# Kernel optimization log

Measured on AMD Instinct MI355X. Metric: run time of the kernel, lower is better.

Reference implementation:

```python
import jax, jax.numpy as jnp
import numpy as np

D = 256; H = 4; DK = D // H
MAX_ATOMS = 13; EDGE_NUM = 78; PAD = 799; K = 20
PREFIX = MAX_ATOMS * 2 + 2 + EDGE_NUM * 4   # 340, tokens that get positional encoding
SEQ = PREFIX + K                             # 360
NPAIR = EDGE_NUM + MAX_ATOMS                 # 91 atom pairs (i,j), j up to max_atoms
DFF = 2048; MSP = 800; B = 256

# ---- static pair / gather index tables (numpy, computed once) ----
def _pairs():
    pi, pj, pe = [], [], []
    for i in range(MAX_ATOMS):
        base = sum(MAX_ATOMS - jj - 1 for jj in range(i))  # getEdgeIdx prefix
        for j in range(i + 1, MAX_ATOMS + 1):
            pi.append(i); pj.append(j); pe.append(base + (j - i) - 1)
    return np.array(pi), np.array(pj), np.array(pe)

PI, PJ, PEI = _pairs()
_eb = MAX_ATOMS * 2 + 2 + 2 * PEI           # edge feature start in encoder output (stride 2)
GIDX = np.stack([2*PI, 2*PI+1, 2*PJ, 2*PJ+1, _eb, _eb+1, _eb+2, _eb+3], axis=1)  # (91,8)
ZMASK = np.ones((NPAIR, 8), np.float32)
ZMASK[PJ == MAX_ATOMS, 4:] = 0.0            # j == max_atoms -> edge slots zeroed
ES = (MAX_ATOMS + 1) * 2 + 4 * PEI          # edge slice start in raw src (stride 4)
EIDX = ES[:, None] + np.arange(4)[None, :]  # (91,4)

def _pe_table():
    pe = np.zeros((PREFIX, D), np.float32)
    pos = np.arange(PREFIX, dtype=np.float64)[:, None]
    ev = np.arange(0, D, 2)
    pe[:, ev] = np.sin(pos / 10000.0 ** (2 * ev / D))
    pe[:, ev + 1] = np.cos(pos / 10000.0 ** (2 * (ev + 1) / D))
    return jnp.asarray(pe)

PETAB = _pe_table()

def _norm(x, a, b):
    mu = x.mean(-1, keepdims=True)
    sd = x.std(-1, keepdims=True, ddof=1)   # torch std is unbiased
    return a * (x - mu) / (sd + 1e-6) + b

def _out_mask(src):
    # vectorized get_pad_mask10; later conditions override earlier ones
    ai = src[:, 2*PI + 1]; aj = src[:, 2*PJ + 1]
    ti = src[:, 2*PI];     tj = src[:, 2*PJ]
    c1 = (ai == 2) | (aj == 2)                                  # -> [0,0,1]
    c2 = (tj == 1) | (ai == 1) | (aj == 1)                      # -> [0,1,1]
    c3 = (ti == PAD) | (tj == PAD) | (ai == 0) | (aj == 0)      # -> [1,1,1]
    c4 = jnp.asarray(PJ < MAX_ATOMS)[None, :] & jnp.any(src[:, EIDX] == 1, axis=-1)
    m111 = c3 | c4
    return jnp.stack([m111, m111 | c2, m111 | c2 | c1], axis=-1)  # (B,91,3) bool


def setup_inputs() -> dict:
    key = jax.random.key(0)
    ks = jax.random.split(key, 12)
    g = lambda k, shape, s=0.02: jax.random.normal(k, shape, jnp.float32) * s
    emb = g(ks[0], (MSP, D), 1.0).at[PAD].set(0.0)  # nn.Embedding zeroes padding row
    return {
        'src': jax.random.randint(ks[1], (B, SEQ), 0, MSP, dtype=jnp.int32),
        'emb': emb,
        'wq': g(ks[2], (D, D)), 'bq': jnp.zeros((D,), jnp.float32),
        'wk': g(ks[3], (D, D)), 'bk': jnp.zeros((D,), jnp.float32),
        'wv': g(ks[4], (D, D)), 'bv': jnp.zeros((D,), jnp.float32),
        'wo': g(ks[5], (D, D)), 'bo': jnp.zeros((D,), jnp.float32),
        'n1a': jnp.ones((D,), jnp.float32), 'n1b': jnp.zeros((D,), jnp.float32),
        'n2a': jnp.ones((D,), jnp.float32), 'n2b': jnp.zeros((D,), jnp.float32),
        'w1': g(ks[6], (D, DFF)), 'b1': jnp.zeros((DFF,), jnp.float32),
        'w2': g(ks[7], (DFF, D)), 'b2': jnp.zeros((D,), jnp.float32),
        'wl': g(ks[8], (8 * D, 3)), 'bl': jnp.zeros((3,), jnp.float32),
    }


def reference(src, emb, wq, bq, wk, bk, wv, bv, wo, bo, n1a, n1b, n2a, n2b,
              w1, b1, w2, b2, wl, bl):
    Bn, S = src.shape
    x = emb[src]                                             # (B,S,D)
    # positional encoding (scale + PE) only on first PREFIX tokens, dropout=eval/no-op
    xp = x[:, :PREFIX] * jnp.sqrt(jnp.float32(D)) + PETAB
    x = jnp.concatenate([xp, x[:, PREFIX:]], axis=1)
    pad = src != PAD                                         # (B,S) query-row mask
    # encoder layer (pre-norm, residual)
    x2 = _norm(x, n1a, n1b)
    def heads(w, b):
        return (x2 @ w + b).reshape(Bn, S, H, DK).transpose(0, 2, 1, 3)
    q, kk, v = heads(wq, bq), heads(wk, bk), heads(wv, bv)
    sc = jnp.einsum('bhqd,bhkd->bhqk', q, kk) / jnp.sqrt(jnp.float32(DK))
    sc = jnp.where(pad[:, None, :, None], sc, jnp.float32(-1e9))  # mask broadcasts over keys
    ctx = jnp.einsum('bhqk,bhkd->bhqd', jax.nn.softmax(sc, axis=-1), v)
    x = x + ctx.transpose(0, 2, 1, 3).reshape(Bn, S, D) @ wo + bo
    x2 = _norm(x, n2a, n2b)
    x = x + jax.nn.relu(x2 @ w1 + b1) @ w2 + b2
    # triangular atom-pair gather + concat, vectorized via static index table
    feat = x[:, GIDX] * jnp.asarray(ZMASK)[None, :, :, None]  # (B,91,8,D)
    logits = feat.reshape(Bn, NPAIR, 8 * D) @ wl + bl         # (B,91,3)
    return jnp.where(_out_mask(src), jnp.float32(-1e9), logits)
```

## Files before the change

kernel.cpp:

```cpp
#include <hip/hip_runtime.h>
#include <hip/hip_bf16.h>
#include <math.h>


using bf16 = __hip_bfloat16;
typedef __attribute__((ext_vector_type(4))) float f32x4;
typedef __attribute__((ext_vector_type(16))) float f32x16;
typedef long long i64;
typedef unsigned char uchar;

static __device__ __forceinline__ float wave_sum64(float v){
  #pragma unroll
  for (int o = 32; o >= 1; o >>= 1) v += __shfl_xor(v, o, 64);
  return v;
}

static __device__ __forceinline__ void gl_lds16(const void* g, void* l){
  __builtin_amdgcn_global_load_lds((const __attribute__((address_space(1))) void*)g,
                                   (__attribute__((address_space(3))) void*)l, 16, 0, 0);
}

static __device__ __forceinline__ unsigned pack2(float a, float b){
  union { bf16 h[2]; unsigned u; } u;
  u.h[0] = __float2bfloat16(a); u.h[1] = __float2bfloat16(b);
  return u.u;
}

static __device__ __forceinline__ uchar f2f8(float v){
  return (uchar)(__builtin_amdgcn_cvt_pk_fp8_f32(v, 0.f, 0, false) & 0xff);
}
static __device__ __forceinline__ unsigned pack4_fp8(float a, float b, float c, float d){
  int v = __builtin_amdgcn_cvt_pk_fp8_f32(a, b, 0, false);
  v = __builtin_amdgcn_cvt_pk_fp8_f32(c, d, v, true);
  return (unsigned)v;
}

static __device__ __forceinline__ float fexp2(float x){
  float r;
  asm("v_exp_f32 %0, %1" : "=v"(r) : "v"(x));
  return r;
}

__global__ __launch_bounds__(256) void cvt_all(
    const float* s0, const float* s1, const float* s2, const float* s3,
    const float* s4, const float* s5,
    uchar* d0, uchar* d1, uchar* d2, uchar* d3, uchar* d4, uchar* d5)
{
  __shared__ float t[32][33];
  const float* srcs[6] = {s0, s1, s2, s3, s4, s5};
  uchar* dsts[6] = {d0, d1, d2, d3, d4, d5};
  const int Ks[6] = {256, 256, 256, 256, 256, 2048};
  const int Ns[6] = {256, 256, 256, 256, 2048, 256};
  const int offs[7] = {0, 64, 128, 192, 256, 768, 1280};
  int bid = blockIdx.x, j = 5;
  #pragma unroll
  for (int q = 4; q >= 0; q--) if (bid < offs[q + 1]) j = q;
  int local = bid - offs[j];
  int K = Ks[j], N = Ns[j];
  const float* src = srcs[j];
  uchar* dst = dsts[j];
  int kt = K >> 5;
  int kb = (local % kt) * 32, nb = (local / kt) * 32;
  int tx = threadIdx.x & 31, ty = threadIdx.x >> 5;
  #pragma unroll
  for (int dy = 0; dy < 32; dy += 8)
    t[ty + dy][tx] = src[(size_t)(kb + ty + dy) * N + nb + tx];
  __syncthreads();
  #pragma unroll
  for (int dy = 0; dy < 32; dy += 8)
    dst[(size_t)(nb + ty + dy) * K + kb + tx] = f2f8(t[tx][ty + dy]);
}

__global__ __launch_bounds__(256) void embed_ln1(
    const int* __restrict__ src, const float* __restrict__ emb,
    const float* __restrict__ na, const float* __restrict__ nb,
    bf16* __restrict__ x, uchar* __restrict__ xn8)
{
  int row  = blockIdx.x * 4 + (threadIdx.x >> 6);
  int lane = threadIdx.x & 63;
  int s = row % 360;
  int tok = src[row];
  float4 v = *(const float4*)(emb + (size_t)tok * 256 + lane * 4);
  float vv[4] = {v.x, v.y, v.z, v.w};
  if (s < 340){
    const float C = (-2.0f / 256.0f) * 13.287712379549449f;
    #pragma unroll
    for (int t = 0; t < 4; t++){
      int c = lane * 4 + t;
      float ang = (float)s * exp2f(C * (float)c);
      float pe = (c & 1) ? cosf(ang) : sinf(ang);
      vv[t] = 16.0f * vv[t] + pe;
    }
  }
  float sum = wave_sum64(vv[0] + vv[1] + vv[2] + vv[3]);
  float mu = sum * (1.0f / 256.0f);
  float d0 = vv[0]-mu, d1 = vv[1]-mu, d2 = vv[2]-mu, d3 = vv[3]-mu;
  float sq = wave_sum64(d0*d0 + d1*d1 + d2*d2 + d3*d3);
  float inv = 1.0f / (sqrtf(sq * (1.0f / 255.0f)) + 1e-6f);
  bf16 xo[4] = { __float2bfloat16(vv[0]), __float2bfloat16(vv[1]),
                 __float2bfloat16(vv[2]), __float2bfloat16(vv[3]) };
  *(uint2*)(x + (size_t)row * 256 + lane * 4) = *(uint2*)xo;
  float4 a4 = *(const float4*)(na + lane * 4);
  float4 b4 = *(const float4*)(nb + lane * 4);
  unsigned u = pack4_fp8(a4.x * d0 * inv + b4.x, a4.y * d1 * inv + b4.y,
                         a4.z * d2 * inv + b4.z, a4.w * d3 * inv + b4.w);
  *(unsigned*)(xn8 + (size_t)row * 256 + lane * 4) = u;
}

__global__ __launch_bounds__(256) void ln_k8(
    const bf16* __restrict__ x, const float* __restrict__ na,
    const float* __restrict__ nb, uchar* __restrict__ xn8)
{
  int row  = blockIdx.x * 4 + (threadIdx.x >> 6);
  int lane = threadIdx.x & 63;
  uint2 raw = *(const uint2*)(x + (size_t)row * 256 + lane * 4);
  bf16* xr = (bf16*)&raw;
  float v0 = __bfloat162float(xr[0]), v1 = __bfloat162float(xr[1]);
  float v2 = __bfloat162float(xr[2]), v3 = __bfloat162float(xr[3]);
  float sum = wave_sum64(v0 + v1 + v2 + v3);
  float mu = sum * (1.0f / 256.0f);
  float d0 = v0-mu, d1 = v1-mu, d2 = v2-mu, d3 = v3-mu;
  float sq = wave_sum64(d0*d0 + d1*d1 + d2*d2 + d3*d3);
  float inv = 1.0f / (sqrtf(sq * (1.0f / 255.0f)) + 1e-6f);
  float4 a4 = *(const float4*)(na + lane * 4);
  float4 b4 = *(const float4*)(nb + lane * 4);
  unsigned u = pack4_fp8(a4.x * d0 * inv + b4.x, a4.y * d1 * inv + b4.y,
                         a4.z * d2 * inv + b4.z, a4.w * d3 * inv + b4.w);
  *(unsigned*)(xn8 + (size_t)row * 256 + lane * 4) = u;
}

template<int MODE>
__global__ __launch_bounds__(256) void gemm_k256(
    const uchar* __restrict__ A, const uchar* __restrict__ Bt,
    const float* __restrict__ bias,
    uchar* __restrict__ out8, bf16* __restrict__ xres,
    int N, int nTiles,
    const float* __restrict__ bq, const float* __restrict__ bk)
{
  __shared__ __align__(16) char smem[65536];
  uchar* As = (uchar*)smem;
  uchar* Bs = (uchar*)(smem + 32768);
  uchar* S8 = (uchar*)smem;
  bf16 (*Cs)[136] = (bf16 (*)[136])smem;
  int chunk = gridDim.x >> 3;
  int bi = (blockIdx.x & 7) * chunk + (blockIdx.x >> 3);
  int m0 = (bi / nTiles) * 128, n0 = (bi % nTiles) * 128;
  int tid = threadIdx.x;
  int wave = tid >> 6, lane = tid & 63;
  int wm = (wave >> 1) * 64, wn = (wave & 1) * 64;
  int r32 = lane & 31, half = lane >> 5;

  #pragma unroll
  for (int j = 0; j < 8; j++){
    int c = j * 256 + tid;
    int row = c >> 4, p = c & 15;
    int sl = (p & 8) | ((p & 7) ^ (row & 7));
    gl_lds16(A  + (size_t)(m0 + row) * 256 + sl * 16, As + (size_t)c * 16);
    gl_lds16(Bt + (size_t)(n0 + row) * 256 + sl * 16, Bs + (size_t)c * 16);
  }

  f32x16 acc[2][2];
  #pragma unroll
  for (int mb = 0; mb < 2; mb++)
    #pragma unroll
    for (int nb = 0; nb < 2; nb++)
      #pragma unroll
      for (int e = 0; e < 16; e++) acc[mb][nb][e] = 0.f;

  __syncthreads();

  #pragma unroll
  for (int c = 0; c < 8; c++){
    int l0 = 2 * c + half;
    i64 alo[2], ahi[2], blo[2], bhi[2];
    #pragma unroll
    for (int mb = 0; mb < 2; mb++){
      int row = wm + mb * 32 + r32;
      int st = (l0 & 8) | ((l0 & 7) ^ (row & 7));
      uint4 v = *(const uint4*)(As + row * 256 + st * 16);
      alo[mb] = *(const i64*)&v.x;  ahi[mb] = *(const i64*)&v.z;
    }
    #pragma unroll
    for (int nb = 0; nb < 2; nb++){
      int row = wn + nb * 32 + r32;
      int st = (l0 & 8) | ((l0 & 7) ^ (row & 7));
      uint4 v = *(const uint4*)(Bs + row * 256 + st * 16);
      blo[nb] = *(const i64*)&v.x;  bhi[nb] = *(const i64*)&v.z;
    }
    #pragma unroll
    for (int mb = 0; mb < 2; mb++)
      #pragma unroll
      for (int nb = 0; nb < 2; nb++){
        if (MODE == 5){
          acc[mb][nb] = __builtin_amdgcn_mfma_f32_32x32x16_fp8_fp8(alo[mb], blo[nb], acc[mb][nb], 0, 0, 0);
          acc[mb][nb] = __builtin_amdgcn_mfma_f32_32x32x16_fp8_fp8(ahi[mb], bhi[nb], acc[mb][nb], 0, 0, 0);
        } else {
          acc[mb][nb] = __builtin_amdgcn_mfma_f32_32x32x16_fp8_fp8(blo[nb], alo[mb], acc[mb][nb], 0, 0, 0);
          acc[mb][nb] = __builtin_amdgcn_mfma_f32_32x32x16_fp8_fp8(bhi[nb], ahi[mb], acc[mb][nb], 0, 0, 0);
        }
      }
  }

  __syncthreads();

  if (MODE == 2 || MODE == 4){
    const int region = (MODE == 4) ? (n0 >> 8) : 0;
    const float* bb = (MODE == 4) ? (region == 0 ? bq : bk) : bias;
    #pragma unroll
    for (int mb = 0; mb < 2; mb++){
      int m_l = wm + mb * 32 + r32;
      #pragma unroll
      for (int nb = 0; nb < 2; nb++)
        #pragma unroll
        for (int g = 0; g < 4; g++){
          int n_l = wn + nb * 32 + g * 8 + half * 4;
          int bidx = (MODE == 4) ? ((n0 & 255) + n_l) : (n0 + n_l);
          float v0 = acc[mb][nb][g * 4 + 0] + bb[bidx + 0];
          float v1 = acc[mb][nb][g * 4 + 1] + bb[bidx + 1];
          float v2 = acc[mb][nb][g * 4 + 2] + bb[bidx + 2];
          float v3 = acc[mb][nb][g * 4 + 3] + bb[bidx + 3];
          if (MODE == 2){
            v0 = fmaxf(v0, 0.f); v1 = fmaxf(v1, 0.f);
            v2 = fmaxf(v2, 0.f); v3 = fmaxf(v3, 0.f);
          }
          *(unsigned*)(S8 + m_l * 136 + n_l) = pack4_fp8(v0, v1, v2, v3);
        }
    }
    __syncthreads();
    int lr = tid >> 1, seg = tid & 1;
    #pragma unroll
    for (int j = 0; j < 4; j++){
      int nl = seg * 64 + j * 16;
      uint2 a = *(uint2*)(S8 + lr * 136 + nl);
      uint2 b = *(uint2*)(S8 + lr * 136 + nl + 8);
      uint4 st = make_uint4(a.x, a.y, b.x, b.y);
      if (MODE == 2){
        *(uint4*)(out8 + (size_t)(m0 + lr) * N + n0 + nl) = st;
      } else {
        int m = m0 + lr;
        int b_ = m / 360, s = m - b_ * 360;
        int nnl = (n0 & 255) + nl;
        int h = nnl >> 6, dk = nnl & 63;
        size_t roff = (region == 1) ? 23592960ull : 0ull;
        *(uint4*)(out8 + roff + ((size_t)(b_ * 4 + h) * 360 + s) * 64 + dk) = st;
      }
    }
  } else if (MODE == 5){
    #pragma unroll
    for (int nb = 0; nb < 2; nb++){
      int n_l = wn + nb * 32 + r32;
      float bv_ = bias[n0 + n_l];
      #pragma unroll
      for (int mb = 0; mb < 2; mb++)
        #pragma unroll
        for (int g = 0; g < 4; g++){
          int m_l = wm + mb * 32 + g * 8 + half * 4;
          *(unsigned*)(S8 + n_l * 136 + m_l) =
              pack4_fp8(acc[mb][nb][g * 4 + 0] + bv_, acc[mb][nb][g * 4 + 1] + bv_,
                        acc[mb][nb][g * 4 + 2] + bv_, acc[mb][nb][g * 4 + 3] + bv_);
        }
    }
    __syncthreads();
    int nn = tid >> 1, part = tid & 1;
    int nnl = n0 + nn;
    int h = nnl >> 6, dk = nnl & 63;
    #pragma unroll
    for (int j0 = 0; j0 < 64; j0 += 8){
      int mm = m0 + part * 64 + j0;
      int b_ = mm / 360, s = mm - b_ * 360;
      uint2 val = *(uint2*)(S8 + nn * 136 + part * 64 + j0);
      *(uint2*)(out8 + ((size_t)((b_ * 4 + h) * 64 + dk)) * 360 + s) = val;
    }
  } else {
    #pragma unroll
    for (int hb = 0; hb < 2; hb++){
      if ((wave >> 1) == hb){
        #pragma unroll
        for (int mb = 0; mb < 2; mb++){
          int ml = mb * 32 + r32;
          #pragma unroll
          for (int nb = 0; nb < 2; nb++)
            #pragma unroll
            for (int g = 0; g < 4; g++){
              int nl0 = wn + nb * 32 + g * 8 + half * 4;
              float v0 = acc[mb][nb][g * 4 + 0] + bias[n0 + nl0 + 0];
              float v1 = acc[mb][nb][g * 4 + 1] + bias[n0 + nl0 + 1];
              float v2 = acc[mb][nb][g * 4 + 2] + bias[n0 + nl0 + 2];
              float v3 = acc[mb][nb][g * 4 + 3] + bias[n0 + nl0 + 3];
              *(unsigned*)(&Cs[ml][nl0])     = pack2(v0, v1);
              *(unsigned*)(&Cs[ml][nl0 + 2]) = pack2(v2, v3);
            }
        }
      }
      __syncthreads();
      int mbase = m0 + hb * 64;
      int lr = tid >> 2, seg = tid & 3;
      bf16* op = xres + (size_t)(mbase + lr) * 256 + n0 + seg * 32;
      #pragma unroll
      for (int j = 0; j < 4; j++){
        uint4 cv = *(uint4*)(&Cs[lr][seg * 32 + j * 8]);
        uint4 xv = *(uint4*)(op + j * 8);
        bf16* ca = (bf16*)&cv; bf16* xa = (bf16*)&xv;
        bf16 o8[8];
        #pragma unroll
        for (int t = 0; t < 8; t++)
          o8[t] = __float2bfloat16(__bfloat162float(ca[t]) + __bfloat162float(xa[t]));
        *(uint4*)(op + j * 8) = *(uint4*)o8;
      }
      __syncthreads();
    }
  }
}

__global__ __launch_bounds__(256) void gemm_ffn2(
    const uchar* __restrict__ A, const uchar* __restrict__ Bt,
    const float* __restrict__ bias, bf16* __restrict__ xres,
    int nTiles)
{
  __shared__ __align__(16) char smem[65536];
  bf16 (*Cs)[136] = (bf16 (*)[136])smem;
  int chunk = gridDim.x >> 3;
  int bi = (blockIdx.x & 7) * chunk + (blockIdx.x >> 3);
  int m0 = (bi / nTiles) * 128, n0 = (bi % nTiles) * 128;
  int tid = threadIdx.x;
  int wave = tid >> 6, lane = tid & 63;
  int wm = (wave >> 1) * 64, wn = (wave & 1) * 64;
  int r32 = lane & 31, half = lane >> 5;

  const uchar* ag[4]; const uchar* bg[4]; int ldst[4];
  #pragma unroll
  for (int j = 0; j < 4; j++){
    int c = j * 256 + tid;
    int row = c >> 3, p = c & 7;
    int sl = p ^ (row & 7);
    ag[j] = A  + (size_t)(m0 + row) * 2048 + sl * 16;
    bg[j] = Bt + (size_t)(n0 + row) * 2048 + sl * 16;
    ldst[j] = c * 16;
  }

  f32x16 acc[2][2];
  #pragma unroll
  for (int mb = 0; mb < 2; mb++)
    #pragma unroll
    for (int nb = 0; nb < 2; nb++)
      #pragma unroll
      for (int e = 0; e < 16; e++) acc[mb][nb][e] = 0.f;

  #pragma unroll
  for (int j = 0; j < 4; j++){
    gl_lds16(ag[j], (uchar*)smem + ldst[j]);
    gl_lds16(bg[j], (uchar*)smem + 32768 + ldst[j]);
  }
  __syncthreads();

  int cur = 0;
  for (int t = 0; t < 16; t++){
    int nxt = cur ^ 1;
    if (t < 15){
      #pragma unroll
      for (int j = 0; j < 4; j++){
        gl_lds16(ag[j] + (t + 1) * 128, (uchar*)smem + nxt * 16384 + ldst[j]);
        gl_lds16(bg[j] + (t + 1) * 128, (uchar*)smem + 32768 + nxt * 16384 + ldst[j]);
      }
    }
    const uchar* Ac = (const uchar*)smem + cur * 16384;
    const uchar* Bc = (const uchar*)smem + 32768 + cur * 16384;
    #pragma unroll
    for (int c = 0; c < 4; c++){
      int l0 = 2 * c + half;
      i64 alo[2], ahi[2], blo[2], bhi[2];
      #pragma unroll
      for (int mb = 0; mb < 2; mb++){
        int row = wm + mb * 32 + r32;
        int st = l0 ^ (row & 7);
        uint4 v = *(const uint4*)(Ac + row * 128 + st * 16);
        alo[mb] = *(const i64*)&v.x;  ahi[mb] = *(const i64*)&v.z;
      }
      #pragma unroll
      for (int nb = 0; nb < 2; nb++){
        int row = wn + nb * 32 + r32;
        int st = l0 ^ (row & 7);
        uint4 v = *(const uint4*)(Bc + row * 128 + st * 16);
        blo[nb] = *(const i64*)&v.x;  bhi[nb] = *(const i64*)&v.z;
      }
      #pragma unroll
      for (int mb = 0; mb < 2; mb++)
        #pragma unroll
        for (int nb = 0; nb < 2; nb++){
          acc[mb][nb] = __builtin_amdgcn_mfma_f32_32x32x16_fp8_fp8(blo[nb], alo[mb], acc[mb][nb], 0, 0, 0);
          acc[mb][nb] = __builtin_amdgcn_mfma_f32_32x32x16_fp8_fp8(bhi[nb], ahi[mb], acc[mb][nb], 0, 0, 0);
        }
    }
    __syncthreads();
    cur ^= 1;
  }

  #pragma unroll
  for (int hb = 0; hb < 2; hb++){
    if ((wave >> 1) == hb){
      #pragma unroll
      for (int mb = 0; mb < 2; mb++){
        int ml = mb * 32 + r32;
        #pragma unroll
        for (int nb = 0; nb < 2; nb++)
          #pragma unroll
          for (int g = 0; g < 4; g++){
            int nl0 = wn + nb * 32 + g * 8 + half * 4;
            float v0 = acc[mb][nb][g * 4 + 0] + bias[n0 + nl0 + 0];
            float v1 = acc[mb][nb][g * 4 + 1] + bias[n0 + nl0 + 1];
            float v2 = acc[mb][nb][g * 4 + 2] + bias[n0 + nl0 + 2];
            float v3 = acc[mb][nb][g * 4 + 3] + bias[n0 + nl0 + 3];
            *(unsigned*)(&Cs[ml][nl0])     = pack2(v0, v1);
            *(unsigned*)(&Cs[ml][nl0 + 2]) = pack2(v2, v3);
          }
      }
    }
    __syncthreads();
    int mbase = m0 + hb * 64;
    int lr = tid >> 2, seg = tid & 3;
    bf16* op = xres + (size_t)(mbase + lr) * 256 + n0 + seg * 32;
    #pragma unroll
    for (int j = 0; j < 4; j++){
      uint4 cv = *(uint4*)(&Cs[lr][seg * 32 + j * 8]);
      uint4 xv = *(uint4*)(op + j * 8);
      bf16* ca = (bf16*)&cv; bf16* xa = (bf16*)&xv;
      bf16 o8[8];
      #pragma unroll
      for (int t = 0; t < 8; t++)
        o8[t] = __float2bfloat16(__bfloat162float(ca[t]) + __bfloat162float(xa[t]));
      *(uint4*)(op + j * 8) = *(uint4*)o8;
    }
    __syncthreads();
  }
}

template<bool TAIL>
static __device__ __forceinline__ void attn_step(
    int kc, const uchar (*Ks)[80], uchar (*Pb)[16][48],
    const uchar* __restrict__ vb, int wave, int r, int qd,
    const i64* qa0, const i64* qa1, float* lsum, f32x4 (*accO)[4])
{
  int krow0 = kc * 32 + r;
  int krow1 = krow0 + 16;
  if (TAIL){ if (krow0 > 359) krow0 = 359; if (krow1 > 359) krow1 = 359; }
  i64 kf00 = *(const i64*)(&Ks[krow0][qd * 8]);
  i64 kf01 = *(const i64*)(&Ks[krow0][32 + qd * 8]);
  i64 kf10 = *(const i64*)(&Ks[krow1][qd * 8]);
  i64 kf11 = *(const i64*)(&Ks[krow1][32 + qd * 8]);
  i64 vf[4];
  #pragma unroll
  for (int dt = 0; dt < 4; dt++)
    vf[dt] = *(const i64*)(vb + (size_t)(dt * 16 + r) * 360 + kc * 32 + qd * 8);

  const float CEXP = 0.18033688011112042f;

  #pragma unroll
  for (int tl = 0; tl < 3; tl++){
    f32x4 z0 = {0.f, 0.f, 0.f, 0.f}, z1 = {0.f, 0.f, 0.f, 0.f};
    z0 = __builtin_amdgcn_mfma_f32_16x16x32_fp8_fp8(kf00, qa0[tl], z0, 0, 0, 0);
    z0 = __builtin_amdgcn_mfma_f32_16x16x32_fp8_fp8(kf01, qa1[tl], z0, 0, 0, 0);
    z1 = __builtin_amdgcn_mfma_f32_16x16x32_fp8_fp8(kf10, qa0[tl], z1, 0, 0, 0);
    z1 = __builtin_amdgcn_mfma_f32_16x16x32_fp8_fp8(kf11, qa1[tl], z1, 0, 0, 0);
    float p0[4], p1[4];
    #pragma unroll
    for (int i = 0; i < 4; i++){
      p0[i] = fexp2(z0[i] * CEXP);
      p1[i] = fexp2(z1[i] * CEXP);
      if (TAIL){
        if (kc * 32 + qd * 4 + i >= 360) p0[i] = 0.f;
        if (kc * 32 + 16 + qd * 4 + i >= 360) p1[i] = 0.f;
      }
      lsum[tl] += p0[i] + p1[i];
    }
    *(unsigned*)(&Pb[wave][r][qd * 4])      = pack4_fp8(p0[0], p0[1], p0[2], p0[3]);
    *(unsigned*)(&Pb[wave][r][16 + qd * 4]) = pack4_fp8(p1[0], p1[1], p1[2], p1[3]);
    asm volatile("s_waitcnt lgkmcnt(0)" ::: "memory");
    i64 pa = *(const i64*)(&Pb[wave][r][qd * 8]);
    #pragma unroll
    for (int dt = 0; dt < 4; dt++)
      accO[tl][dt] = __builtin_amdgcn_mfma_f32_16x16x32_fp8_fp8(pa, vf[dt], accO[tl][dt], 0, 0, 0);
    asm volatile("s_waitcnt lgkmcnt(0)" ::: "memory");
  }
}

__global__ __launch_bounds__(512) void attn5(
    const uchar* __restrict__ q, const uchar* __restrict__ kk, const uchar* __restrict__ vt,
    const int* __restrict__ src, uchar* __restrict__ ctx8)
{
  __shared__ __align__(16) uchar smem[34944];
  uchar (*Ks)[80]     = (uchar (*)[80])smem;
  uchar (*Pb)[16][48] = (uchar (*)[16][48])(smem + 28800);
  int bh = blockIdx.x;
  int b = bh >> 2, h = bh & 3;
  int wave = threadIdx.x >> 6, lane = threadIdx.x & 63;
  int r = lane & 15, qd = lane >> 4;
  const uchar* qb = q  + (size_t)bh * 360 * 64;
  const uchar* kb = kk + (size_t)bh * 360 * 64;
  const uchar* vb = vt + (size_t)bh * 64 * 360;
  const int* srow = src + b * 360;

  for (int c = threadIdx.x; c < 1440; c += 512){
    int row = c >> 2, g = c & 3;
    *(uint4*)(&Ks[row][g * 16]) = *(const uint4*)(kb + row * 64 + g * 16);
  }
  __syncthreads();

  i64 qa0[3], qa1[3];
  float lsum[3];
  f32x4 accO[3][4];
  #pragma unroll
  for (int tl = 0; tl < 3; tl++){
    int qt = wave * 3 + tl;
    int qg = qt * 16 + r;
    int qrow = qg > 359 ? 359 : qg;
    bool qp = (qg < 360) && (srow[qg] == 799);
    i64 a0 = *(const i64*)(qb + qrow * 64 + qd * 8);
    i64 a1 = *(const i64*)(qb + qrow * 64 + 32 + qd * 8);
    qa0[tl] = qp ? 0 : a0;
    qa1[tl] = qp ? 0 : a1;
    lsum[tl] = 0.f;
    #pragma unroll
    for (int dt = 0; dt < 4; dt++) accO[tl][dt] = (f32x4){0.f, 0.f, 0.f, 0.f};
  }

  for (int kc = 0; kc < 11; kc++)
    attn_step<false>(kc, Ks, Pb, vb, wave, r, qd, qa0, qa1, lsum, accO);
  attn_step<true>(11, Ks, Pb, vb, wave, r, qd, qa0, qa1, lsum, accO);

  __syncthreads();
  uchar* Cw = smem + wave * 1280;

  #pragma unroll
  for (int tl = 0; tl < 3; tl++){
    float ls = lsum[tl];
    ls += __shfl_xor(ls, 16, 64);
    ls += __shfl_xor(ls, 32, 64);
    float invl = 1.0f / ls;
    #pragma unroll
    for (int dt = 0; dt < 4; dt++)
      *(unsigned*)(Cw + r * 80 + dt * 16 + qd * 4) =
          pack4_fp8(accO[tl][dt][0] * invl, accO[tl][dt][1] * invl,
                    accO[tl][dt][2] * invl, accO[tl][dt][3] * invl);
    asm volatile("s_waitcnt lgkmcnt(0)" ::: "memory");
    int qt = wave * 3 + tl;
    int qglob = qt * 16 + r;
    if (qglob < 360)
      *(uint4*)(ctx8 + ((size_t)(b * 360 + qglob)) * 256 + h * 64 + qd * 16) =
          *(uint4*)(Cw + r * 80 + qd * 16);
    asm volatile("s_waitcnt lgkmcnt(0)" ::: "memory");
  }
}

__global__ __launch_bounds__(256) void head_k(
    const bf16* __restrict__ x, const int* __restrict__ src,
    const float* __restrict__ wl, const float* __restrict__ bl,
    float* __restrict__ out)
{
  __shared__ bf16 Xs[192][264];
  int b = blockIdx.x;
  int tid = threadIdx.x;
  int wave = tid >> 6, lane = tid & 63;
  int g = lane >> 3, sub = lane & 7;

  const bf16* xb = x + (size_t)b * 360 * 256;
  for (int it = 0; it < 24; it++){
    int idx = tid + it * 256;
    int row = idx >> 5, col = idx & 31;
    *(uint4*)(&Xs[row][col * 8]) = *(const uint4*)(xb + row * 256 + col * 8);
  }

  float wv[96];
  {
    const float4* wr4 = (const float4*)(wl + (size_t)(g * 256 + sub * 32) * 3);
    #pragma unroll
    for (int c = 0; c < 24; c++) *(float4*)(&wv[c * 4]) = wr4[c];
  }
  float bl0 = bl[0], bl1 = bl[1], bl2 = bl[2];
  const int* sr = src + b * 360;
  __syncthreads();

  for (int p = wave; p < 91; p += 4){
    int i = 0, rem = p;
    while (rem >= 13 - i){ rem -= 13 - i; i++; }
    int j = i + 1 + rem;
    int base = 12 * i - (i * (i - 1)) / 2;
    int pe = base + (j - i) - 1;
    int eb = 28 + 2 * pe;

    int idxg;
    if (g == 0) idxg = 2 * i;
    else if (g == 1) idxg = 2 * i + 1;
    else if (g == 2) idxg = 2 * j;
    else if (g == 3) idxg = 2 * j + 1;
    else idxg = eb + (g - 4);
    bool zm = !(g >= 4 && j == 13);

    uint4 xv[4];
    #pragma unroll
    for (int c = 0; c < 4; c++) xv[c] = *(uint4*)(&Xs[idxg][sub * 32 + c * 8]);
    const bf16* xa = (const bf16*)xv;
    float a0 = 0.f, a1 = 0.f, a2 = 0.f;
    #pragma unroll
    for (int t = 0; t < 32; t++){
      float f = zm ? __bfloat162float(xa[t]) : 0.0f;
      a0 += f * wv[t * 3 + 0];
      a1 += f * wv[t * 3 + 1];
      a2 += f * wv[t * 3 + 2];
    }
    #pragma unroll
    for (int o = 1; o < 64; o <<= 1){
      a0 += __shfl_xor(a0, o, 64);
      a1 += __shfl_xor(a1, o, 64);
      a2 += __shfl_xor(a2, o, 64);
    }
    if (lane == 0){
      int ti = sr[2 * i], ai = sr[2 * i + 1], tj = sr[2 * j], aj = sr[2 * j + 1];
      bool c1 = (ai == 2) || (aj == 2);
      bool c2 = (tj == 1) || (ai == 1) || (aj == 1);
      bool c3 = (ti == 799) || (tj == 799) || (ai == 0) || (aj == 0);
      bool c4 = false;
      if (j < 13){
        int es = 28 + 4 * pe;
        c4 = (sr[es] == 1) || (sr[es + 1] == 1) || (sr[es + 2] == 1) || (sr[es + 3] == 1);
      }
      bool m1 = c3 || c4, m2 = m1 || c2, m3 = m2 || c1;
      float* op = out + ((size_t)b * 91 + p) * 3;
      op[0] = m1 ? -1.0e9f : (a0 + bl0);
      op[1] = m2 ? -1.0e9f : (a1 + bl1);
      op[2] = m3 ? -1.0e9f : (a2 + bl2);
    }
  }
}

extern "C" void kernel_launch(void* const* d_in, const int* in_sizes, int n_in,
                              void* d_out, int out_size, void* d_ws, size_t ws_size,
                              hipStream_t stream)
{
  const int*   src = (const int*)  d_in[0];
  const float* emb = (const float*)d_in[1];
  const float* wq  = (const float*)d_in[2];  const float* bq = (const float*)d_in[3];
  const float* wk  = (const float*)d_in[4];  const float* bk = (const float*)d_in[5];
  const float* wv  = (const float*)d_in[6];  const float* bv = (const float*)d_in[7];
  const float* wo  = (const float*)d_in[8];  const float* bo = (const float*)d_in[9];
  const float* n1a = (const float*)d_in[10]; const float* n1b = (const float*)d_in[11];
  const float* n2a = (const float*)d_in[12]; const float* n2b = (const float*)d_in[13];
  const float* w1  = (const float*)d_in[14]; const float* b1 = (const float*)d_in[15];
  const float* w2  = (const float*)d_in[16]; const float* b2 = (const float*)d_in[17];
  const float* wl  = (const float*)d_in[18]; const float* bl = (const float*)d_in[19];
  float* out = (float*)d_out;

  if (ws_size < 191365120ull) return;

  char* ws = (char*)d_ws;
  bf16*  x    = (bf16*)(ws);
  uchar* xn8  = (uchar*)(ws + 47185920ull);
  char*  R    = ws + 70778880ull;
  uchar* q8   = (uchar*)(R);
  uchar* vt8  = (uchar*)(R + 47185920ull);
  uchar* h8   = (uchar*)(R);
  char*  wC   = ws + 165150720ull;
  uchar* wqkv8 = (uchar*)(wC);
  uchar* wo8   = (uchar*)(wC + 196608);
  uchar* w1f8T = (uchar*)(wC + 262144);
  uchar* w2f8T = (uchar*)(wC + 786432);

  cvt_all<<<1280, 256, 0, stream>>>(wq, wk, wv, wo, w1, w2,
                                    wqkv8, wqkv8 + 65536, wqkv8 + 131072,
                                    wo8, w1f8T, w2f8T);

  embed_ln1<<<23040, 256, 0, stream>>>(src, emb, n1a, n1b, x, xn8);

  gemm_k256<4><<<2880, 256, 0, stream>>>(xn8, wqkv8, nullptr, q8, nullptr,
                                         512, 4, bq, bk);
  gemm_k256<5><<<1440, 256, 0, stream>>>(xn8, wqkv8 + 131072, bv, vt8, nullptr,
                                         256, 2, nullptr, nullptr);

  attn5<<<1024, 512, 0, stream>>>(q8, q8 + 23592960ull, vt8, src, xn8 );

  gemm_k256<3><<<1440, 256, 0, stream>>>(xn8, wo8, bo, nullptr, x,
                                         256, 2, nullptr, nullptr);

  ln_k8<<<23040, 256, 0, stream>>>(x, n2a, n2b, xn8);

  for (int mc = 0; mc < 2; mc++){
    const uchar* xnc = xn8 + (size_t)mc * 46080 * 256;
    bf16* xc = x + (size_t)mc * 46080 * 256;
    gemm_k256<2><<<5760, 256, 0, stream>>>(xnc, w1f8T, b1, h8, nullptr,
                                           2048, 16, nullptr, nullptr);
    gemm_ffn2<<<720, 256, 0, stream>>>(h8, w2f8T, b2, xc, 2);
  }

  head_k<<<256, 256, 0, stream>>>(x, src, wl, bl, out);
}
```

Baseline: 553.8 us.

## Fuse FFN up and down projections into one kernel keeping hidden tile in LDS

Replaces the two-kernel FFN (W1 GEMM writing an fp8 hidden tensor to global memory, then a W2 GEMM reading it back) with a single kernel. Each 512-thread block owns 128 rows, loops over 8 chunks of 256 hidden units, computes the ReLU'd hidden chunk into LDS, and immediately accumulates it against the matching W2 slice. This removes the global round-trip of the large hidden activation and two launches, but uses 160KB of dynamic LDS (one block per CU) and drops the double-buffered prefetch, so weight loads are no longer overlapped with MFMA work.

```diff
diff --git a/kernel.cpp b/kernel.cpp
--- a/kernel.cpp
+++ b/kernel.cpp
@@ -203,9 +203,9 @@
 
   __syncthreads();
 
-  if (MODE == 2 || MODE == 4){
-    const int region = (MODE == 4) ? (n0 >> 8) : 0;
-    const float* bb = (MODE == 4) ? (region == 0 ? bq : bk) : bias;
+  if (MODE == 4){
+    const int region = n0 >> 8;
+    const float* bb = (region == 0 ? bq : bk);
     #pragma unroll
     for (int mb = 0; mb < 2; mb++){
       int m_l = wm + mb * 32 + r32;
@@ -214,15 +214,11 @@
         #pragma unroll
         for (int g = 0; g < 4; g++){
           int n_l = wn + nb * 32 + g * 8 + half * 4;
-          int bidx = (MODE == 4) ? ((n0 & 255) + n_l) : (n0 + n_l);
+          int bidx = (n0 & 255) + n_l;
           float v0 = acc[mb][nb][g * 4 + 0] + bb[bidx + 0];
           float v1 = acc[mb][nb][g * 4 + 1] + bb[bidx + 1];
           float v2 = acc[mb][nb][g * 4 + 2] + bb[bidx + 2];
           float v3 = acc[mb][nb][g * 4 + 3] + bb[bidx + 3];
-          if (MODE == 2){
-            v0 = fmaxf(v0, 0.f); v1 = fmaxf(v1, 0.f);
-            v2 = fmaxf(v2, 0.f); v3 = fmaxf(v3, 0.f);
-          }
           *(unsigned*)(S8 + m_l * 136 + n_l) = pack4_fp8(v0, v1, v2, v3);
         }
     }
@@ -234,16 +230,12 @@
       uint2 a = *(uint2*)(S8 + lr * 136 + nl);
       uint2 b = *(uint2*)(S8 + lr * 136 + nl + 8);
       uint4 st = make_uint4(a.x, a.y, b.x, b.y);
-      if (MODE == 2){
-        *(uint4*)(out8 + (size_t)(m0 + lr) * N + n0 + nl) = st;
-      } else {
-        int m = m0 + lr;
-        int b_ = m / 360, s = m - b_ * 360;
-        int nnl = (n0 & 255) + nl;
-        int h = nnl >> 6, dk = nnl & 63;
-        size_t roff = (region == 1) ? 23592960ull : 0ull;
-        *(uint4*)(out8 + roff + ((size_t)(b_ * 4 + h) * 360 + s) * 64 + dk) = st;
-      }
+      int m = m0 + lr;
+      int b_ = m / 360, s = m - b_ * 360;
+      int nnl = (n0 & 255) + nl;
+      int h = nnl >> 6, dk = nnl & 63;
+      size_t roff = (region == 1) ? 23592960ull : 0ull;
+      *(uint4*)(out8 + roff + ((size_t)(b_ * 4 + h) * 360 + s) * 64 + dk) = st;
     }
   } else if (MODE == 5){
     #pragma unroll
@@ -312,125 +304,163 @@
   }
 }
 
-__global__ __launch_bounds__(256) void gemm_ffn2(
-    const uchar* __restrict__ A, const uchar* __restrict__ Bt,
-    const float* __restrict__ bias, bf16* __restrict__ xres,
-    int nTiles)
-{
-  __shared__ __align__(16) char smem[65536];
-  bf16 (*Cs)[136] = (bf16 (*)[136])smem;
-  int chunk = gridDim.x >> 3;
-  int bi = (blockIdx.x & 7) * chunk + (blockIdx.x >> 3);
-  int m0 = (bi / nTiles) * 128, n0 = (bi % nTiles) * 128;
+__global__ __launch_bounds__(512) void gemm_ffn(
+    const uchar* __restrict__ A, const uchar* __restrict__ W1t,
+    const uchar* __restrict__ W2t, const float* __restrict__ b1,
+    const float* __restrict__ b2, bf16* __restrict__ xres)
+{
+  extern __shared__ __align__(16) char sm[];
+  const int W1OFF = 32768, W2OFF = 98304;
+  int bi = (blockIdx.x & 7) * 90 + (blockIdx.x >> 3);
+  int m0 = bi * 128;
   int tid = threadIdx.x;
   int wave = tid >> 6, lane = tid & 63;
-  int wm = (wave >> 1) * 64, wn = (wave & 1) * 64;
+  int wm = (wave & 1) * 64, wn = (wave >> 1) * 64;
   int r32 = lane & 31, half = lane >> 5;
 
-  const uchar* ag[4]; const uchar* bg[4]; int ldst[4];
   #pragma unroll
   for (int j = 0; j < 4; j++){
-    int c = j * 256 + tid;
-    int row = c >> 3, p = c & 7;
-    int sl = p ^ (row & 7);
-    ag[j] = A  + (size_t)(m0 + row) * 2048 + sl * 16;
-    bg[j] = Bt + (size_t)(n0 + row) * 2048 + sl * 16;
-    ldst[j] = c * 16;
-  }
-
-  f32x16 acc[2][2];
+    int c = j * 512 + tid;
+    int row = c >> 4, p = c & 15;
+    int sl = (p & 8) | ((p & 7) ^ (row & 7));
+    gl_lds16(A + (size_t)(m0 + row) * 256 + sl * 16, sm + c * 16);
+  }
+
+  f32x16 acc2[2][2];
   #pragma unroll
   for (int mb = 0; mb < 2; mb++)
     #pragma unroll
     for (int nb = 0; nb < 2; nb++)
       #pragma unroll
-      for (int e = 0; e < 16; e++) acc[mb][nb][e] = 0.f;
-
-  #pragma unroll
-  for (int j = 0; j < 4; j++){
-    gl_lds16(ag[j], (uchar*)smem + ldst[j]);
-    gl_lds16(bg[j], (uchar*)smem + 32768 + ldst[j]);
-  }
-  __syncthreads();
-
-  int cur = 0;
-  for (int t = 0; t < 16; t++){
-    int nxt = cur ^ 1;
-    if (t < 15){
-      #pragma unroll
-      for (int j = 0; j < 4; j++){
-        gl_lds16(ag[j] + (t + 1) * 128, (uchar*)smem + nxt * 16384 + ldst[j]);
-        gl_lds16(bg[j] + (t + 1) * 128, (uchar*)smem + 32768 + nxt * 16384 + ldst[j]);
-      }
-    }
-    const uchar* Ac = (const uchar*)smem + cur * 16384;
-    const uchar* Bc = (const uchar*)smem + 32768 + cur * 16384;
-    #pragma unroll
-    for (int c = 0; c < 4; c++){
+      for (int e = 0; e < 16; e++) acc2[mb][nb][e] = 0.f;
+
+  for (int s = 0; s < 8; s++){
+    #pragma unroll
+    for (int j = 0; j < 8; j++){
+      int c = j * 512 + tid;
+      int row = c >> 4, p = c & 15;
+      int sl = (p & 8) | ((p & 7) ^ (row & 7));
+      gl_lds16(W1t + (size_t)((s << 8) + row) * 256 + sl * 16, sm + W1OFF + c * 16);
+      gl_lds16(W2t + (size_t)row * 2048 + (s << 8) + sl * 16, sm + W2OFF + c * 16);
+    }
+    __syncthreads();
+
+    f32x16 acc1[2][2];
+    #pragma unroll
+    for (int mb = 0; mb < 2; mb++)
+      #pragma unroll
+      for (int nb = 0; nb < 2; nb++)
+        #pragma unroll
+        for (int e = 0; e < 16; e++) acc1[mb][nb][e] = 0.f;
+    #pragma unroll
+    for (int c = 0; c < 8; c++){
       int l0 = 2 * c + half;
-      i64 alo[2], ahi[2], blo[2], bhi[2];
+      i64 alo[2], ahi[2], wlo[2], whi[2];
       #pragma unroll
       for (int mb = 0; mb < 2; mb++){
         int row = wm + mb * 32 + r32;
-        int st = l0 ^ (row & 7);
-        uint4 v = *(const uint4*)(Ac + row * 128 + st * 16);
+        int st = (l0 & 8) | ((l0 & 7) ^ (row & 7));
+        uint4 v = *(const uint4*)(sm + row * 256 + st * 16);
         alo[mb] = *(const i64*)&v.x;  ahi[mb] = *(const i64*)&v.z;
       }
       #pragma unroll
       for (int nb = 0; nb < 2; nb++){
         int row = wn + nb * 32 + r32;
-        int st = l0 ^ (row & 7);
-        uint4 v = *(const uint4*)(Bc + row * 128 + st * 16);
-        blo[nb] = *(const i64*)&v.x;  bhi[nb] = *(const i64*)&v.z;
+        int st = (l0 & 8) | ((l0 & 7) ^ (row & 7));
+        uint4 v = *(const uint4*)(sm + W1OFF + row * 256 + st * 16);
+        wlo[nb] = *(const i64*)&v.x;  whi[nb] = *(const i64*)&v.z;
       }
       #pragma unroll
       for (int mb = 0; mb < 2; mb++)
         #pragma unroll
         for (int nb = 0; nb < 2; nb++){
-          acc[mb][nb] = __builtin_amdgcn_mfma_f32_32x32x16_fp8_fp8(blo[nb], alo[mb], acc[mb][nb], 0, 0, 0);
-          acc[mb][nb] = __builtin_amdgcn_mfma_f32_32x32x16_fp8_fp8(bhi[nb], ahi[mb], acc[mb][nb], 0, 0, 0);
+          acc1[mb][nb] = __builtin_amdgcn_mfma_f32_32x32x16_fp8_fp8(wlo[nb], alo[mb], acc1[mb][nb], 0, 0, 0);
+          acc1[mb][nb] = __builtin_amdgcn_mfma_f32_32x32x16_fp8_fp8(whi[nb], ahi[mb], acc1[mb][nb], 0, 0, 0);
         }
     }
     __syncthreads();
-    cur ^= 1;
-  }
-
-  #pragma unroll
-  for (int hb = 0; hb < 2; hb++){
-    if ((wave >> 1) == hb){
+
+    #pragma unroll
+    for (int mb = 0; mb < 2; mb++){
+      int m = wm + mb * 32 + r32;
+      #pragma unroll
+      for (int nb = 0; nb < 2; nb++)
+        #pragma unroll
+        for (int g = 0; g < 4; g++){
+          int n_l = wn + nb * 32 + g * 8 + half * 4;
+          float4 bv = *(const float4*)(b1 + (s << 8) + n_l);
+          float v0 = fmaxf(acc1[mb][nb][g * 4 + 0] + bv.x, 0.f);
+          float v1 = fmaxf(acc1[mb][nb][g * 4 + 1] + bv.y, 0.f);
+          float v2 = fmaxf(acc1[mb][nb][g * 4 + 2] + bv.z, 0.f);
+          float v3 = fmaxf(acc1[mb][nb][g * 4 + 3] + bv.w, 0.f);
+          int p_l = n_l >> 4;
+          int sl = (p_l & 8) | ((p_l & 7) ^ (m & 7));
+          *(unsigned*)(sm + W1OFF + m * 256 + sl * 16 + (n_l & 15)) =
+              pack4_fp8(v0, v1, v2, v3);
+        }
+    }
+    __syncthreads();
+
+    #pragma unroll
+    for (int c = 0; c < 8; c++){
+      int l0 = 2 * c + half;
+      i64 hlo[2], hhi[2], wlo[2], whi[2];
       #pragma unroll
       for (int mb = 0; mb < 2; mb++){
-        int ml = mb * 32 + r32;
+        int row = wm + mb * 32 + r32;
+        int st = (l0 & 8) | ((l0 & 7) ^ (row & 7));
+        uint4 v = *(const uint4*)(sm + W1OFF + row * 256 + st * 16);
+        hlo[mb] = *(const i64*)&v.x;  hhi[mb] = *(const i64*)&v.z;
+      }
+      #pragma unroll
+      for (int nb = 0; nb < 2; nb++){
+        int row = wn + nb * 32 + r32;
+        int st = (l0 & 8) | ((l0 & 7) ^ (row & 7));
+        uint4 v = *(const uint4*)(sm + W2OFF + row * 256 + st * 16);
+        wlo[nb] = *(const i64*)&v.x;  whi[nb] = *(const i64*)&v.z;
+      }
+      #pragma unroll
+      for (int mb = 0; mb < 2; mb++)
         #pragma unroll
-        for (int nb = 0; nb < 2; nb++)
-          #pragma unroll
-          for (int g = 0; g < 4; g++){
-            int nl0 = wn + nb * 32 + g * 8 + half * 4;
-            float v0 = acc[mb][nb][g * 4 + 0] + bias[n0 + nl0 + 0];
-            float v1 = acc[mb][nb][g * 4 + 1] + bias[n0 + nl0 + 1];
-            float v2 = acc[mb][nb][g * 4 + 2] + bias[n0 + nl0 + 2];
-            float v3 = acc[mb][nb][g * 4 + 3] + bias[n0 + nl0 + 3];
-            *(unsigned*)(&Cs[ml][nl0])     = pack2(v0, v1);
-            *(unsigned*)(&Cs[ml][nl0 + 2]) = pack2(v2, v3);
-          }
-      }
+        for (int nb = 0; nb < 2; nb++){
+          acc2[mb][nb] = __builtin_amdgcn_mfma_f32_32x32x16_fp8_fp8(wlo[nb], hlo[mb], acc2[mb][nb], 0, 0, 0);
+          acc2[mb][nb] = __builtin_amdgcn_mfma_f32_32x32x16_fp8_fp8(whi[nb], hhi[mb], acc2[mb][nb], 0, 0, 0);
+        }
     }
     __syncthreads();
-    int mbase = m0 + hb * 64;
-    int lr = tid >> 2, seg = tid & 3;
-    bf16* op = xres + (size_t)(mbase + lr) * 256 + n0 + seg * 32;
-    #pragma unroll
-    for (int j = 0; j < 4; j++){
-      uint4 cv = *(uint4*)(&Cs[lr][seg * 32 + j * 8]);
-      uint4 xv = *(uint4*)(op + j * 8);
-      bf16* ca = (bf16*)&cv; bf16* xa = (bf16*)&xv;
-      bf16 o8[8];
-      #pragma unroll
-      for (int t = 0; t < 8; t++)
-        o8[t] = __float2bfloat16(__bfloat162float(ca[t]) + __bfloat162float(xa[t]));
-      *(uint4*)(op + j * 8) = *(uint4*)o8;
-    }
-    __syncthreads();
+  }
+
+  bf16 (*Cs)[136] = (bf16 (*)[136])(sm + W1OFF);
+  #pragma unroll
+  for (int mb = 0; mb < 2; mb++){
+    int ml = wm + mb * 32 + r32;
+    #pragma unroll
+    for (int nb = 0; nb < 2; nb++)
+      #pragma unroll
+      for (int g = 0; g < 4; g++){
+        int nl0 = wn + nb * 32 + g * 8 + half * 4;
+        float4 bv = *(const float4*)(b2 + nl0);
+        float v0 = acc2[mb][nb][g * 4 + 0] + bv.x;
+        float v1 = acc2[mb][nb][g * 4 + 1] + bv.y;
+        float v2 = acc2[mb][nb][g * 4 + 2] + bv.z;
+        float v3 = acc2[mb][nb][g * 4 + 3] + bv.w;
+        *(unsigned*)(&Cs[ml][nl0])     = pack2(v0, v1);
+        *(unsigned*)(&Cs[ml][nl0 + 2]) = pack2(v2, v3);
+      }
+  }
+  __syncthreads();
+  int lr = tid >> 2, seg = tid & 3;
+  bf16* op = xres + (size_t)(m0 + lr) * 256 + seg * 64;
+  #pragma unroll
+  for (int j = 0; j < 8; j++){
+    uint4 cv = *(uint4*)(&Cs[lr][seg * 64 + j * 8]);
+    uint4 xv = *(uint4*)(op + j * 8);
+    bf16* ca = (bf16*)&cv; bf16* xa = (bf16*)&xv;
+    bf16 o8[8];
+    #pragma unroll
+    for (int t = 0; t < 8; t++)
+      o8[t] = __float2bfloat16(__bfloat162float(ca[t]) + __bfloat162float(xa[t]));
+    *(uint4*)(op + j * 8) = *(uint4*)o8;
   }
 }
 
@@ -657,7 +687,6 @@
   char*  R    = ws + 70778880ull;
   uchar* q8   = (uchar*)(R);
   uchar* vt8  = (uchar*)(R + 47185920ull);
-  uchar* h8   = (uchar*)(R);
   char*  wC   = ws + 165150720ull;
   uchar* wqkv8 = (uchar*)(wC);
   uchar* wo8   = (uchar*)(wC + 196608);
@@ -682,13 +711,7 @@
 
   ln_k8<<<23040, 256, 0, stream>>>(x, n2a, n2b, xn8);
 
-  for (int mc = 0; mc < 2; mc++){
-    const uchar* xnc = xn8 + (size_t)mc * 46080 * 256;
-    bf16* xc = x + (size_t)mc * 46080 * 256;
-    gemm_k256<2><<<5760, 256, 0, stream>>>(xnc, w1f8T, b1, h8, nullptr,
-                                           2048, 16, nullptr, nullptr);
-    gemm_ffn2<<<720, 256, 0, stream>>>(h8, w2f8T, b2, xc, 2);
-  }
+  gemm_ffn<<<720, 512, 163840, stream>>>(xn8, w1f8T, w2f8T, b1, b2, x);
 
   head_k<<<256, 256, 0, stream>>>(x, src, wl, bl, out);
 }
```

After: 533.1 us. 1.04x faster.
